# Kernel optimization log

Measured on AMD Instinct MI355X. Metric: run time of the kernel, lower is better.

Reference implementation:

```python
import jax, jax.numpy as jnp
import numpy as np

MARGIN = 0.2
ENCODER_STRIDE = 320


def setup_inputs() -> dict:
    key = jax.random.key(0)
    k1, k2, k3, k4 = jax.random.split(key, 4)
    B, D, T, NC = 8, 512, 2048, 4096
    student_features = jax.random.normal(k1, (B, D, T), dtype=jnp.float32)
    codebook = jax.random.normal(k2, (NC, D), dtype=jnp.float32)
    teacher_codes = jax.random.randint(k3, (B, T), 0, NC, dtype=jnp.int64)
    lengths = jax.random.randint(k4, (B,), 0, T * ENCODER_STRIDE, dtype=jnp.int64)
    return {
        "student_features": student_features,
        "teacher_codes": teacher_codes,
        "codebook": codebook,
        "lengths": lengths,
    }


def reference(student_features, teacher_codes, codebook, lengths):
    B, D, T = student_features.shape
    # frame-level valid mask: (B, T)
    frame_lengths = lengths // ENCODER_STRIDE
    mask = (jnp.arange(T)[None, :] < frame_lengths[:, None]).astype(student_features.dtype)

    # (B*T, D) flattened student vectors
    z = jnp.transpose(student_features, (0, 2, 1)).reshape(-1, D)

    # Euclidean cdist via ||z||^2 + ||c||^2 - 2 z c^T (matmul form, like torch.cdist)
    sq = (
        jnp.sum(z * z, axis=-1, keepdims=True)
        + jnp.sum(codebook * codebook, axis=-1)[None, :]
        - 2.0 * jnp.einsum("nd,cd->nc", z, codebook)
    )
    dists = jnp.sqrt(jnp.maximum(sq, 1e-12))  # (B*T, num_codes)

    teacher_flat = teacher_codes.reshape(-1)
    rows = jnp.arange(teacher_flat.shape[0])
    pos_dist = dists[rows, teacher_flat]
    # exclude the target code, then min over codebook
    dists_for_neg = dists.at[rows, teacher_flat].set(jnp.inf)
    neg_dist = jnp.min(dists_for_neg, axis=1)

    triplet = jax.nn.relu(pos_dist.reshape(B, T) - neg_dist.reshape(B, T) + MARGIN)
    loss = jnp.sum(triplet * mask) / (jnp.sum(mask) + 1e-8)
    return loss
```

## Files before the change

kernel.cpp:

```cpp
#include <hip/hip_runtime.h>
#include <hip/hip_bf16.h>

typedef __bf16 bf16x8 __attribute__((ext_vector_type(8)));
typedef float f32x4 __attribute__((ext_vector_type(4)));
typedef int v8i __attribute__((ext_vector_type(8)));

#define NB 8
#define ND 512
#define NT 2048
#define NCODES 4096
#define NM (NB * NT)
#define MARGIN_F 0.2f
#define ENC_STRIDE 320


static __device__ inline unsigned short f2bf(float v) {
    __hip_bfloat16 h = __float2bfloat16(v);
    return __builtin_bit_cast(unsigned short, h);
}

static __device__ inline void async_copy16(const void* g, void* l) {
    __builtin_amdgcn_global_load_lds(
        (const __attribute__((address_space(1))) unsigned int*)g,
        (__attribute__((address_space(3))) unsigned int*)l, 16, 0, 0);
}

__global__ void student_prep(const float* __restrict__ sf, unsigned char* __restrict__ Zq,
                             unsigned short* __restrict__ Zrm) {
    __shared__ float tile[128][65];
    const int b = blockIdx.z;
    const int t0 = blockIdx.x * 64;
    const int d0 = blockIdx.y * 128;
    const int tid = threadIdx.x;
    const float* src = sf + (size_t)b * ND * NT;
#pragma unroll
    for (int it = 0; it < 8; it++) {
        int idx = it * 256 + tid;
        int d = idx >> 4, t4 = (idx & 15) * 4;
        float4 v = *(const float4*)(src + (size_t)(d0 + d) * NT + t0 + t4);
        tile[d][t4] = v.x; tile[d][t4 + 1] = v.y; tile[d][t4 + 2] = v.z; tile[d][t4 + 3] = v.w;
    }
    __syncthreads();
    const int wave = tid >> 6, lane = tid & 63, l15 = lane & 15, kq = lane >> 4;
    const int m0 = b * NT + t0;
    {
        const int trow = wave * 16 + l15;
        unsigned char q[32];
#pragma unroll
        for (int j = 0; j < 32; j += 2) {
            float a = tile[kq * 32 + j][trow];
            float c = tile[kq * 32 + j + 1][trow];
            int p = __builtin_amdgcn_cvt_pk_fp8_f32(a, c, 0, false);
            q[j] = (unsigned char)(p & 0xFF);
            q[j + 1] = (unsigned char)((p >> 8) & 0xFF);
        }
        const int M_ = m0 >> 7, rg = ((m0 >> 4) & 7) + wave, K_ = d0 >> 7;
        char* base = (char*)Zq + ((size_t)((M_ * 4 + K_) * 8 + rg)) * 2048;
        *(uint4*)(base + lane * 16) = *(uint4*)&q[0];
        *(uint4*)(base + 1024 + lane * 16) = *(uint4*)&q[16];
    }
    {
        int t = tid >> 2;
#pragma unroll
        for (int it = 0; it < 8; it++) {
            int d = (tid & 3) * 4 + it * 16;
            ushort4 o;
            o.x = f2bf(tile[d][t]); o.y = f2bf(tile[d + 1][t]);
            o.z = f2bf(tile[d + 2][t]); o.w = f2bf(tile[d + 3][t]);
            *(ushort4*)(Zrm + (size_t)(m0 + t) * ND + d0 + d) = o;
        }
    }
}

__global__ void codebook_fp8(const float* __restrict__ cb, unsigned char* __restrict__ Cq) {
    const int tid = threadIdx.x, wave = tid >> 6, lane = tid & 63, l15 = lane & 15, kq = lane >> 4;
    const int r0 = blockIdx.x * 64, K_ = blockIdx.y;
    const int row = r0 + wave * 16 + l15;
    const float* srcr = cb + (size_t)row * ND + K_ * 128 + kq * 32;
    unsigned char q[32];
#pragma unroll
    for (int j4 = 0; j4 < 8; j4++) {
        float4 v = *(const float4*)(srcr + j4 * 4);
        int p0 = __builtin_amdgcn_cvt_pk_fp8_f32(v.x, v.y, 0, false);
        int p1 = __builtin_amdgcn_cvt_pk_fp8_f32(v.z, v.w, 0, false);
        q[j4 * 4 + 0] = (unsigned char)(p0 & 0xFF);
        q[j4 * 4 + 1] = (unsigned char)((p0 >> 8) & 0xFF);
        q[j4 * 4 + 2] = (unsigned char)(p1 & 0xFF);
        q[j4 * 4 + 3] = (unsigned char)((p1 >> 8) & 0xFF);
    }
    const int N_ = r0 >> 7, rg = ((r0 >> 4) & 7) + wave;
    char* base = (char*)Cq + ((size_t)((N_ * 4 + K_) * 8 + rg)) * 2048;
    *(uint4*)(base + lane * 16) = *(uint4*)&q[0];
    *(uint4*)(base + 1024 + lane * 16) = *(uint4*)&q[16];
}

__global__ void cnorm_k(const float* __restrict__ cb, float* __restrict__ cnorm) {
    int wave = threadIdx.x >> 6, lane = threadIdx.x & 63;
    int row = blockIdx.x * 4 + wave;
    const float* src = cb + (size_t)row * ND + lane * 8;
    float s = 0.0f;
#pragma unroll
    for (int i = 0; i < 2; i++) {
        float4 v = *(const float4*)(src + i * 4);
        s += v.x * v.x + v.y * v.y + v.z * v.z + v.w * v.w;
    }
#pragma unroll
    for (int off = 1; off < 64; off <<= 1) s += __shfl_xor(s, off);
    if (lane == 0) cnorm[row] = s;
}

__global__ __launch_bounds__(256, 2) void triplet_main(
    const unsigned char* __restrict__ Zq, const unsigned char* __restrict__ Cq,
    const float* __restrict__ cnorm, const int* __restrict__ teacher,
    unsigned int* __restrict__ minq) {
    __shared__ __align__(16) unsigned char As[16384];
    __shared__ __align__(16) unsigned char Bs[16384];

    const int M_ = blockIdx.x;
    const int nq = blockIdx.y;
    const int m0 = M_ * 128;
    const int tid = threadIdx.x;
    const int wave = tid >> 6, lane = tid & 63;
    const int wr = wave >> 1, wc = wave & 1;
    const int l15 = lane & 15, quad = lane >> 4;

    unsigned int minu[4][4];
    int tch[4][4];
#pragma unroll
    for (int mi = 0; mi < 4; mi++)
#pragma unroll
        for (int r = 0; r < 4; r++) {
            minu[mi][r] = 0xFFFFFFFFu;
            tch[mi][r] = teacher[m0 + wr * 64 + mi * 16 + quad * 4 + r];
        }

    const char* gA0 = (const char*)Zq + (size_t)M_ * 4 * 16384 + wave * 4096 + lane * 16;
    char* lA = (char*)As + wave * 4096;
    char* lB = (char*)Bs + wave * 4096;

    for (int nt = 0; nt < 4; nt++) {
        const int N_ = nq * 4 + nt;
        const int n0 = N_ * 128;
        const char* gA = gA0;
        const char* gB = (const char*)Cq + (size_t)N_ * 4 * 16384 + wave * 4096 + lane * 16;
        f32x4 acc[4][4] = {};

        for (int kt = 0; kt < 4; kt++) {
#pragma unroll
            for (int i = 0; i < 4; i++) {
                async_copy16(gA + i * 1024, lA + i * 1024);
                async_copy16(gB + i * 1024, lB + i * 1024);
            }
            gA += 16384; gB += 16384;
            __syncthreads();

            v8i av[4], bv[4];
#pragma unroll
            for (int mi = 0; mi < 4; mi++) {
                int rg = wr * 4 + mi;
                union { uint4 q[2]; v8i v; } u;
                u.q[0] = *(const uint4*)(As + rg * 2048 + lane * 16);
                u.q[1] = *(const uint4*)(As + rg * 2048 + 1024 + lane * 16);
                av[mi] = u.v;
            }
#pragma unroll
            for (int ni = 0; ni < 4; ni++) {
                int rg = wc * 4 + ni;
                union { uint4 q[2]; v8i v; } u;
                u.q[0] = *(const uint4*)(Bs + rg * 2048 + lane * 16);
                u.q[1] = *(const uint4*)(Bs + rg * 2048 + 1024 + lane * 16);
                bv[ni] = u.v;
            }
#pragma unroll
            for (int mi = 0; mi < 4; mi++)
#pragma unroll
                for (int ni = 0; ni < 4; ni++)
                    acc[mi][ni] = __builtin_amdgcn_mfma_scale_f32_16x16x128_f8f6f4(
                        av[mi], bv[ni], acc[mi][ni], 0, 0,
                        0, 0x7F7F7F7F, 0, 0x7F7F7F7F);
            __syncthreads();
        }

        float cn[4]; int col[4];
#pragma unroll
        for (int ni = 0; ni < 4; ni++) {
            col[ni] = n0 + wc * 64 + ni * 16 + l15;
            cn[ni] = cnorm[col[ni]];
        }
#pragma unroll
        for (int mi = 0; mi < 4; mi++)
#pragma unroll
            for (int r = 0; r < 4; r++) {
                int t = tch[mi][r];
#pragma unroll
                for (int ni = 0; ni < 4; ni++) {
                    float val = fmaxf(fmaf(-2.0f, acc[mi][ni][r], cn[ni]), 0.0f);
                    unsigned int u = (__builtin_bit_cast(unsigned int, val) & 0xFFFFF000u)
                                     | (unsigned int)col[ni];
                    u = (col[ni] == t) ? 0xFFFFFFFFu : u;
                    minu[mi][r] = min(minu[mi][r], u);
                }
            }
    }

    const int slot = nq * 2 + wc;
#pragma unroll
    for (int mi = 0; mi < 4; mi++)
#pragma unroll
        for (int r = 0; r < 4; r++) {
            unsigned int u = minu[mi][r];
#pragma unroll
            for (int off = 1; off < 16; off <<= 1) u = min(u, (unsigned int)__shfl_xor((int)u, off));
            if (l15 == 0) {
                int m = m0 + wr * 64 + mi * 16 + quad * 4 + r;
                minq[(size_t)slot * NM + m] = u;
            }
        }
}

__global__ void refine(const unsigned short* __restrict__ Zrm, const float* __restrict__ cb,
                       const unsigned int* __restrict__ minq, const int* __restrict__ teacher,
                       const int* __restrict__ lengths, float* __restrict__ blocksums) {
    const int tid = threadIdx.x, wave = tid >> 6, lane = tid & 63;
    const int m = blockIdx.x * 4 + wave;
    unsigned int u = minq[(size_t)(lane & 15) * NM + m];
    u = min(u, (unsigned int)__shfl_xor((int)u, 1));
    u = min(u, (unsigned int)__shfl_xor((int)u, 2));
    u = min(u, (unsigned int)__shfl_xor((int)u, 4));
    u = min(u, (unsigned int)__shfl_xor((int)u, 8));
    const int ng = (int)(u & 0xFFFu);
    const int tch = teacher[m];
    bf16x8 z8 = *(const bf16x8*)(Zrm + (size_t)m * ND + lane * 8);
    const float* cn_ = cb + (size_t)ng * ND + lane * 8;
    const float* ct_ = cb + (size_t)tch * ND + lane * 8;
    float an = 0.0f, at = 0.0f;
#pragma unroll
    for (int i = 0; i < 2; i++) {
        float4 vn = *(const float4*)(cn_ + i * 4);
        float4 vt = *(const float4*)(ct_ + i * 4);
        float z0 = (float)z8[i * 4 + 0], z1 = (float)z8[i * 4 + 1];
        float z2 = (float)z8[i * 4 + 2], z3 = (float)z8[i * 4 + 3];
        float d;
        d = z0 - vn.x; an += d * d;  d = z0 - vt.x; at += d * d;
        d = z1 - vn.y; an += d * d;  d = z1 - vt.y; at += d * d;
        d = z2 - vn.z; an += d * d;  d = z2 - vt.z; at += d * d;
        d = z3 - vn.w; an += d * d;  d = z3 - vt.w; at += d * d;
    }
#pragma unroll
    for (int off = 1; off < 64; off <<= 1) {
        an += __shfl_xor(an, off);
        at += __shfl_xor(at, off);
    }
    __shared__ float red[4];
    if (lane == 0) {
        float negd = sqrtf(fmaxf(an, 1e-12f));
        float posd = sqrtf(fmaxf(at, 1e-12f));
        float tri = fmaxf(posd - negd + MARGIN_F, 0.0f);
        int t = m & (NT - 1);
        int b = m >> 11;
        int flen = lengths[b] / ENC_STRIDE;
        red[wave] = (t < flen) ? tri : 0.0f;
    }
    __syncthreads();
    if (tid == 0) blocksums[blockIdx.x] = red[0] + red[1] + red[2] + red[3];
}

__global__ void finalize(const float* __restrict__ blocksums, const int* __restrict__ lengths,
                         float* __restrict__ out) {
    int tid = threadIdx.x;
    float s = 0.0f;
#pragma unroll
    for (int i = 0; i < 16; i++) s += blocksums[tid + i * 256];
#pragma unroll
    for (int off = 1; off < 64; off <<= 1) s += __shfl_xor(s, off);
    __shared__ float red[4];
    int lane = tid & 63, w = tid >> 6;
    if (lane == 0) red[w] = s;
    __syncthreads();
    if (tid == 0) {
        float cnt = 0.0f;
        for (int b = 0; b < NB; b++) cnt += (float)(lengths[b] / ENC_STRIDE);
        out[0] = (red[0] + red[1] + red[2] + red[3]) / (cnt + 1e-8f);
    }
}

extern "C" void kernel_launch(void* const* d_in, const int* in_sizes, int n_in,
                              void* d_out, int out_size, void* d_ws, size_t ws_size,
                              hipStream_t stream) {
    const float* sf = (const float*)d_in[0];
    const int* teacher = (const int*)d_in[1];
    const float* cb = (const float*)d_in[2];
    const int* lengths = (const int*)d_in[3];

    char* ws = (char*)d_ws;
    unsigned char* Zq = (unsigned char*)(ws);
    unsigned char* Cq = (unsigned char*)(ws + 8388608);
    unsigned short* Zrm = (unsigned short*)(ws + 10485760);
    float* cnorm = (float*)(ws + 27262976);
    unsigned int* minq = (unsigned int*)(ws + 27279360);
    float* blocksums = (float*)(ws + 28327936);

    student_prep<<<dim3(NT / 64, ND / 128, NB), 256, 0, stream>>>(sf, Zq, Zrm);
    codebook_fp8<<<dim3(NCODES / 64, 4), 256, 0, stream>>>(cb, Cq);
    cnorm_k<<<NCODES / 4, 256, 0, stream>>>(cb, cnorm);
    triplet_main<<<dim3(128, 8), 256, 0, stream>>>(Zq, Cq, cnorm, teacher, minq);
    refine<<<NM / 4, 256, 0, stream>>>(Zrm, cb, minq, teacher, lengths, blocksums);
    finalize<<<1, 256, 0, stream>>>(blocksums, lengths, (float*)d_out);
}
```

Measured before the change: 151.0 us.

## Fuse codebook prep with norms, keep student tile resident, stream codebook via registers

```diff
diff --git a/kernel.cpp b/kernel.cpp
--- a/kernel.cpp
+++ b/kernel.cpp
@@ -72,15 +72,22 @@
     }
 }
 
-__global__ void codebook_fp8(const float* __restrict__ cb, unsigned char* __restrict__ Cq) {
-    const int tid = threadIdx.x, wave = tid >> 6, lane = tid & 63, l15 = lane & 15, kq = lane >> 4;
-    const int r0 = blockIdx.x * 64, K_ = blockIdx.y;
-    const int row = r0 + wave * 16 + l15;
-    const float* srcr = cb + (size_t)row * ND + K_ * 128 + kq * 32;
+__global__ void codebook_prep(const float* __restrict__ cb, unsigned char* __restrict__ Cq,
+                              float* __restrict__ cnorm, float* __restrict__ accum,
+                              unsigned int* __restrict__ ticket) {
+    const int tid = threadIdx.x;
+    if (blockIdx.x == 0 && tid == 0) { *accum = 0.0f; *ticket = 0u; }
+    const int wave = tid >> 6, lane = tid & 63, l15 = lane & 15, kq = lane >> 4;
+    const int r0 = blockIdx.x * 16;
+    const int row = r0 + l15;
+    const int K_ = wave;
+    const float* src = cb + (size_t)row * ND + K_ * 128 + kq * 32;
     unsigned char q[32];
+    float s = 0.0f;
 #pragma unroll
     for (int j4 = 0; j4 < 8; j4++) {
-        float4 v = *(const float4*)(srcr + j4 * 4);
+        float4 v = *(const float4*)(src + j4 * 4);
+        s += v.x * v.x + v.y * v.y + v.z * v.z + v.w * v.w;
         int p0 = __builtin_amdgcn_cvt_pk_fp8_f32(v.x, v.y, 0, false);
         int p1 = __builtin_amdgcn_cvt_pk_fp8_f32(v.z, v.w, 0, false);
         q[j4 * 4 + 0] = (unsigned char)(p0 & 0xFF);
@@ -88,33 +95,23 @@
         q[j4 * 4 + 2] = (unsigned char)(p1 & 0xFF);
         q[j4 * 4 + 3] = (unsigned char)((p1 >> 8) & 0xFF);
     }
-    const int N_ = r0 >> 7, rg = ((r0 >> 4) & 7) + wave;
+    const int N_ = r0 >> 7, rg = (r0 >> 4) & 7;
     char* base = (char*)Cq + ((size_t)((N_ * 4 + K_) * 8 + rg)) * 2048;
     *(uint4*)(base + lane * 16) = *(uint4*)&q[0];
     *(uint4*)(base + 1024 + lane * 16) = *(uint4*)&q[16];
-}
-
-__global__ void cnorm_k(const float* __restrict__ cb, float* __restrict__ cnorm) {
-    int wave = threadIdx.x >> 6, lane = threadIdx.x & 63;
-    int row = blockIdx.x * 4 + wave;
-    const float* src = cb + (size_t)row * ND + lane * 8;
-    float s = 0.0f;
-#pragma unroll
-    for (int i = 0; i < 2; i++) {
-        float4 v = *(const float4*)(src + i * 4);
-        s += v.x * v.x + v.y * v.y + v.z * v.z + v.w * v.w;
-    }
-#pragma unroll
-    for (int off = 1; off < 64; off <<= 1) s += __shfl_xor(s, off);
-    if (lane == 0) cnorm[row] = s;
+    s += __shfl_xor(s, 16);
+    s += __shfl_xor(s, 32);
+    __shared__ float red[4][16];
+    if (lane < 16) red[wave][l15] = s;
+    __syncthreads();
+    if (tid < 16) cnorm[r0 + tid] = red[0][tid] + red[1][tid] + red[2][tid] + red[3][tid];
 }
 
 __global__ __launch_bounds__(256, 2) void triplet_main(
     const unsigned char* __restrict__ Zq, const unsigned char* __restrict__ Cq,
     const float* __restrict__ cnorm, const int* __restrict__ teacher,
     unsigned int* __restrict__ minq) {
-    __shared__ __align__(16) unsigned char As[16384];
-    __shared__ __align__(16) unsigned char Bs[16384];
+    __shared__ __align__(16) unsigned char As[65536];
 
     const int M_ = blockIdx.x;
     const int nq = blockIdx.y;
@@ -124,6 +121,13 @@
     const int wr = wave >> 1, wc = wave & 1;
     const int l15 = lane & 15, quad = lane >> 4;
 
+    {
+        const char* gA = (const char*)Zq + (size_t)M_ * 65536 + wave * 16384 + lane * 16;
+        char* lA = (char*)As + wave * 16384;
+#pragma unroll
+        for (int i = 0; i < 16; i++) async_copy16(gA + i * 1024, lA + i * 1024);
+    }
+
     unsigned int minu[4][4];
     int tch[4][4];
 #pragma unroll
@@ -133,52 +137,53 @@
             minu[mi][r] = 0xFFFFFFFFu;
             tch[mi][r] = teacher[m0 + wr * 64 + mi * 16 + quad * 4 + r];
         }
-
-    const char* gA0 = (const char*)Zq + (size_t)M_ * 4 * 16384 + wave * 4096 + lane * 16;
-    char* lA = (char*)As + wave * 4096;
-    char* lB = (char*)Bs + wave * 4096;
+    __syncthreads();
 
     for (int nt = 0; nt < 4; nt++) {
         const int N_ = nq * 4 + nt;
         const int n0 = N_ * 128;
-        const char* gA = gA0;
-        const char* gB = (const char*)Cq + (size_t)N_ * 4 * 16384 + wave * 4096 + lane * 16;
+        const char* tB = (const char*)Cq + (size_t)N_ * 4 * 16384 + (wc * 4) * 2048 + lane * 16;
         f32x4 acc[4][4] = {};
-
+        uint4 bq[4][2];
+#pragma unroll
+        for (int ni = 0; ni < 4; ni++) {
+            bq[ni][0] = *(const uint4*)(tB + ni * 2048);
+            bq[ni][1] = *(const uint4*)(tB + ni * 2048 + 1024);
+        }
+#pragma unroll
         for (int kt = 0; kt < 4; kt++) {
-#pragma unroll
-            for (int i = 0; i < 4; i++) {
-                async_copy16(gA + i * 1024, lA + i * 1024);
-                async_copy16(gB + i * 1024, lB + i * 1024);
-            }
-            gA += 16384; gB += 16384;
-            __syncthreads();
-
-            v8i av[4], bv[4];
+            uint4 bn[4][2];
+            if (kt < 3) {
+                const char* nB = tB + (kt + 1) * 16384;
+#pragma unroll
+                for (int ni = 0; ni < 4; ni++) {
+                    bn[ni][0] = *(const uint4*)(nB + ni * 2048);
+                    bn[ni][1] = *(const uint4*)(nB + ni * 2048 + 1024);
+                }
+            }
+            v8i av[4];
 #pragma unroll
             for (int mi = 0; mi < 4; mi++) {
-                int rg = wr * 4 + mi;
                 union { uint4 q[2]; v8i v; } u;
-                u.q[0] = *(const uint4*)(As + rg * 2048 + lane * 16);
-                u.q[1] = *(const uint4*)(As + rg * 2048 + 1024 + lane * 16);
+                const unsigned char* fb = As + ((kt * 8) + (wr * 4 + mi)) * 2048 + lane * 16;
+                u.q[0] = *(const uint4*)fb;
+                u.q[1] = *(const uint4*)(fb + 1024);
                 av[mi] = u.v;
             }
 #pragma unroll
-            for (int ni = 0; ni < 4; ni++) {
-                int rg = wc * 4 + ni;
-                union { uint4 q[2]; v8i v; } u;
-                u.q[0] = *(const uint4*)(Bs + rg * 2048 + lane * 16);
-                u.q[1] = *(const uint4*)(Bs + rg * 2048 + 1024 + lane * 16);
-                bv[ni] = u.v;
-            }
-#pragma unroll
             for (int mi = 0; mi < 4; mi++)
 #pragma unroll
-                for (int ni = 0; ni < 4; ni++)
+                for (int ni = 0; ni < 4; ni++) {
+                    union { uint4 q[2]; v8i v; } u;
+                    u.q[0] = bq[ni][0]; u.q[1] = bq[ni][1];
                     acc[mi][ni] = __builtin_amdgcn_mfma_scale_f32_16x16x128_f8f6f4(
-                        av[mi], bv[ni], acc[mi][ni], 0, 0,
+                        av[mi], u.v, acc[mi][ni], 0, 0,
                         0, 0x7F7F7F7F, 0, 0x7F7F7F7F);
-            __syncthreads();
+                }
+            if (kt < 3) {
+#pragma unroll
+                for (int ni = 0; ni < 4; ni++) { bq[ni][0] = bn[ni][0]; bq[ni][1] = bn[ni][1]; }
+            }
         }
 
         float cn[4]; int col[4];
@@ -218,9 +223,10 @@
         }
 }
 
-__global__ void refine(const unsigned short* __restrict__ Zrm, const float* __restrict__ cb,
-                       const unsigned int* __restrict__ minq, const int* __restrict__ teacher,
-                       const int* __restrict__ lengths, float* __restrict__ blocksums) {
+__global__ void refine_final(const unsigned short* __restrict__ Zrm, const float* __restrict__ cb,
+                             const unsigned int* __restrict__ minq, const int* __restrict__ teacher,
+                             const int* __restrict__ lengths, float* __restrict__ accum,
+                             unsigned int* __restrict__ ticket, float* __restrict__ out) {
     const int tid = threadIdx.x, wave = tid >> 6, lane = tid & 63;
     const int m = blockIdx.x * 4 + wave;
     unsigned int u = minq[(size_t)(lane & 15) * NM + m];
@@ -262,25 +268,16 @@
         red[wave] = (t < flen) ? tri : 0.0f;
     }
     __syncthreads();
-    if (tid == 0) blocksums[blockIdx.x] = red[0] + red[1] + red[2] + red[3];
-}
-
-__global__ void finalize(const float* __restrict__ blocksums, const int* __restrict__ lengths,
-                         float* __restrict__ out) {
-    int tid = threadIdx.x;
-    float s = 0.0f;
-#pragma unroll
-    for (int i = 0; i < 16; i++) s += blocksums[tid + i * 256];
-#pragma unroll
-    for (int off = 1; off < 64; off <<= 1) s += __shfl_xor(s, off);
-    __shared__ float red[4];
-    int lane = tid & 63, w = tid >> 6;
-    if (lane == 0) red[w] = s;
-    __syncthreads();
     if (tid == 0) {
-        float cnt = 0.0f;
-        for (int b = 0; b < NB; b++) cnt += (float)(lengths[b] / ENC_STRIDE);
-        out[0] = (red[0] + red[1] + red[2] + red[3]) / (cnt + 1e-8f);
+        atomicAdd(accum, red[0] + red[1] + red[2] + red[3]);
+        __threadfence();
+        unsigned int old = atomicAdd(ticket, 1u);
+        if (old == (unsigned int)(gridDim.x - 1)) {
+            float total = atomicAdd(accum, 0.0f);
+            float cnt = 0.0f;
+            for (int b = 0; b < NB; b++) cnt += (float)(lengths[b] / ENC_STRIDE);
+            out[0] = total / (cnt + 1e-8f);
+        }
     }
 }
 
@@ -298,12 +295,12 @@
     unsigned short* Zrm = (unsigned short*)(ws + 10485760);
     float* cnorm = (float*)(ws + 27262976);
     unsigned int* minq = (unsigned int*)(ws + 27279360);
-    float* blocksums = (float*)(ws + 28327936);
+    float* accum = (float*)(ws + 28327936);
+    unsigned int* ticket = (unsigned int*)(ws + 28327940);
 
     student_prep<<<dim3(NT / 64, ND / 128, NB), 256, 0, stream>>>(sf, Zq, Zrm);
-    codebook_fp8<<<dim3(NCODES / 64, 4), 256, 0, stream>>>(cb, Cq);
-    cnorm_k<<<NCODES / 4, 256, 0, stream>>>(cb, cnorm);
+    codebook_prep<<<NCODES / 16, 256, 0, stream>>>(cb, Cq, cnorm, accum, ticket);
     triplet_main<<<dim3(128, 8), 256, 0, stream>>>(Zq, Cq, cnorm, teacher, minq);
-    refine<<<NM / 4, 256, 0, stream>>>(Zrm, cb, minq, teacher, lengths, blocksums);
-    finalize<<<1, 256, 0, stream>>>(blocksums, lengths, (float*)d_out);
-}
+    refine_final<<<NM / 4, 256, 0, stream>>>(Zrm, cb, minq, teacher, lengths, accum, ticket,
+                                             (float*)d_out);
+}
```

New measurement: 288.1 us. 90.8% more time.
